# Kernel optimization log

Measured on AMD Instinct MI355X. Metric: run time of the kernel, lower is better.

Reference implementation:

```python
import jax, jax.numpy as jnp
import numpy as np

N = 50000
E = 800000
T = 5            # towers
F = 10           # in_num / F_in per tower (divide_input=False)
F_OUT = 2        # out_channels // towers
G = 64           # number of graphs in the batch
L = 2            # conv layers
BN_EPS = 1e-5
STD_EPS = 1e-5


def setup_inputs() -> dict:
    key = jax.random.key(0)
    ks = jax.random.split(key, 24)
    s = 0.1
    inp = {
        'x': jax.random.normal(ks[0], (N, F), jnp.float32),
        'edge_emb': jax.random.normal(ks[1], (4, F), jnp.float32) * s,
        'mlp1_w1': jax.random.normal(ks[2], (F, 5), jnp.float32) * s,
        'mlp1_b1': jnp.zeros((5,), jnp.float32),
        'mlp1_w2': jax.random.normal(ks[3], (5, F), jnp.float32) * s,
        'mlp1_b2': jnp.zeros((F,), jnp.float32),
        'enc_w': jax.random.normal(ks[4], (L, F, F), jnp.float32) * s,
        'enc_b': jnp.zeros((L, F), jnp.float32),
        'pre_w': jax.random.normal(ks[5], (L, T, 3 * F, F), jnp.float32) * s,
        'pre_b': jnp.zeros((L, T, F), jnp.float32),
        'post_w': jax.random.normal(ks[6], (L, T, 13 * F, F_OUT), jnp.float32) * s,
        'post_b': jnp.zeros((L, T, F_OUT), jnp.float32),
        'lin_w': jax.random.normal(ks[7], (L, F, F), jnp.float32) * s,
        'lin_b': jnp.zeros((L, F), jnp.float32),
        'bn_gamma': jnp.ones((L, F), jnp.float32),
        'bn_beta': jnp.zeros((L, F), jnp.float32),
        'mlp2_w1': jax.random.normal(ks[8], (F, 5), jnp.float32) * s,
        'mlp2_b1': jnp.zeros((5,), jnp.float32),
        'mlp2_w2': jax.random.normal(ks[9], (5, 1), jnp.float32) * s,
        'mlp2_b2': jnp.zeros((1,), jnp.float32),
        'edge_index': jax.random.randint(ks[10], (2, E), 0, N, jnp.int64),
        'edge_attr': jax.random.randint(ks[11], (E,), 0, 4, jnp.int64),
        'batch': jnp.sort(jax.random.randint(ks[12], (N,), 0, G, jnp.int64)),
    }
    return inp


def reference(x, edge_emb, mlp1_w1, mlp1_b1, mlp1_w2, mlp1_b2,
              enc_w, enc_b, pre_w, pre_b, post_w, post_b, lin_w, lin_b,
              bn_gamma, bn_beta, mlp2_w1, mlp2_b1, mlp2_w2, mlp2_b2,
              edge_index, edge_attr, batch):
    src, dst = edge_index[0], edge_index[1]
    # mlp1: 10 -> 5 -> 10
    h = jax.nn.relu(x @ mlp1_w1 + mlp1_b1) @ mlp1_w2 + mlp1_b2  # [N, F]
    ea = edge_emb[edge_attr]  # [E, F] edge embedding lookup

    # in-degree at target nodes, PNA degree statistics
    deg = jax.ops.segment_sum(jnp.ones((src.shape[0],), h.dtype), dst, num_segments=N)
    d = jnp.clip(deg, 1.0)
    avg_log = jnp.mean(jnp.log(deg + 1.0))  # avg_deg['log'] from degree distribution
    log_d = jnp.log(d + 1.0)
    amp = (log_d / avg_log)[:, None, None]
    att = (avg_log / log_d)[:, None, None]
    has_in = (deg > 0)[:, None, None]
    inv_d = (1.0 / d)[:, None, None]

    for l in range(L):
        e = ea @ enc_w[l] + enc_b[l]  # [E, F]
        # message = pre_nn(cat(x_i, x_j, edge_attr)) per tower (x shared across towers)
        msg_in = jnp.concatenate([h[dst], h[src], e], axis=-1)  # [E, 3F]
        m = jnp.einsum('ef,tfo->eto', msg_in, pre_w[l]) + pre_b[l]  # [E, T, F]
        mean = jax.ops.segment_sum(m, dst, num_segments=N) * inv_d
        mean2 = jax.ops.segment_sum(m * m, dst, num_segments=N) * inv_d
        std = jnp.sqrt(jax.nn.relu(mean2 - mean * mean) + STD_EPS)
        mn = jnp.where(has_in, jax.ops.segment_min(m, dst, num_segments=N), 0.0)
        mx = jnp.where(has_in, jax.ops.segment_max(m, dst, num_segments=N), 0.0)
        agg = jnp.concatenate([mean, mn, mx, std], axis=-1)  # [N, T, 4F]
        agg = jnp.concatenate([agg, agg * amp, agg * att], axis=-1)  # [N, T, 12F]
        xt = jnp.broadcast_to(h[:, None, :], (h.shape[0], T, F))
        o = jnp.concatenate([xt, agg], axis=-1)  # [N, T, 13F]
        o = jnp.einsum('ntf,tfo->nto', o, post_w[l]) + post_b[l]  # [N, T, F_OUT]
        o = o.reshape(o.shape[0], T * F_OUT) @ lin_w[l] + lin_b[l]  # [N, F]
        # train-mode BatchNorm over nodes
        mu = jnp.mean(o, axis=0)
        var = jnp.var(o, axis=0)
        o = (o - mu) / jnp.sqrt(var + BN_EPS) * bn_gamma[l] + bn_beta[l]
        h = jax.nn.relu(o)

    g = jax.ops.segment_sum(h, batch, num_segments=G)  # global_add_pool -> [G, F]
    out = jax.nn.relu(g @ mlp2_w1 + mlp2_b1) @ mlp2_w2 + mlp2_b2  # [G, 1]
    return out
```

## Files before the change

kernel.cpp:

```cpp
#include <hip/hip_runtime.h>
#include <math.h>

#define N_NODES 50000
#define N_EDGES 800000
#define G_GRAPHS 64
#define CONV_BLOCKS 2048
#define BSTRIDE 64

#define WAVE_SYNC() asm volatile("s_waitcnt lgkmcnt(0)" ::: "memory")
#define RFL(v) __builtin_amdgcn_readfirstlane(v)

__global__ void k_mlp1(const float* __restrict__ x,
                       const float* __restrict__ w1, const float* __restrict__ b1,
                       const float* __restrict__ w2, const float* __restrict__ b2,
                       float* __restrict__ h,
                       int* __restrict__ cnt,
                       float* __restrict__ bn_part, float* __restrict__ g,
                       float* __restrict__ avg_log,
                       const float* __restrict__ edge_emb,
                       const float* __restrict__ enc_w, const float* __restrict__ enc_b,
                       const float* __restrict__ pre_w, float* __restrict__ encm,
                       float* __restrict__ u) {
  __shared__ float eo[2][4][10];
  __shared__ float sw[500];
  int tid = threadIdx.x;
  int n = blockIdx.x * blockDim.x + tid;
  if (n < 1280) bn_part[n] = 0.f;
  if (n < G_GRAPHS * 10) g[n] = 0.f;
  if (n == 0) avg_log[0] = 0.f;

  bool act = n < N_NODES;
  float hr[10];
  if (act) {
    cnt[n] = 0;
    float xv[10];
#pragma unroll
    for (int k = 0; k < 10; k++) xv[k] = x[n * 10 + k];
    float hid[5];
#pragma unroll
    for (int j = 0; j < 5; j++) {
      float a = b1[j];
#pragma unroll
      for (int k = 0; k < 10; k++) a += xv[k] * w1[k * 5 + j];
      hid[j] = fmaxf(a, 0.f);
    }
#pragma unroll
    for (int f = 0; f < 10; f++) {
      float a = b2[f];
#pragma unroll
      for (int j = 0; j < 5; j++) a += hid[j] * w2[j * 10 + f];
      hr[f] = a;
      h[n * 10 + f] = a;
    }
  }
  for (int j = tid; j < 500; j += 256) {
    int t = j / 100, k = (j / 10) % 10, f = j % 10;
    sw[j] = pre_w[(t * 30 + 10 + k) * 10 + f];
  }
  if (blockIdx.x == 0) {
    for (int i = tid; i < 80; i += 256) {
      int l = i / 40; int a = (i / 10) % 4; int k = i % 10;
      float s = enc_b[l * 10 + k];
      for (int j = 0; j < 10; j++) s += edge_emb[a * 10 + j] * enc_w[(l * 10 + j) * 10 + k];
      eo[l][a][k] = s;
    }
  }
  __syncthreads();
  if (blockIdx.x == 0) {
    for (int i = tid; i < 400; i += 256) {
      int l = i / 200; int a = (i / 50) % 4; int t = (i / 10) % 5; int f = i % 10;
      float s = 0.f;
      for (int k = 0; k < 10; k++) s += eo[l][a][k] * pre_w[((l * 5 + t) * 30 + 20 + k) * 10 + f];
      encm[i] = s;
    }
  }
  if (act) {
    float2* up = (float2*)(u + n * 50);
#pragma unroll
    for (int c0 = 0; c0 < 25; c0++) {
      int ca = 2 * c0, cb = 2 * c0 + 1;
      int ta = ca / 10, fa = ca % 10, tb = cb / 10, fb = cb % 10;
      float a = 0.f, b = 0.f;
#pragma unroll
      for (int k = 0; k < 10; k++) {
        a += hr[k] * sw[ta * 100 + fa + k * 10];
        b += hr[k] * sw[tb * 100 + fb + k * 10];
      }
      up[c0] = make_float2(a, b);
    }
  }
}

__global__ void k_scatter(const int* __restrict__ src, const int* __restrict__ dst,
                          const int* __restrict__ attr,
                          int* __restrict__ cnt, int* __restrict__ epk) {
  int e = blockIdx.x * blockDim.x + threadIdx.x;
  if (e >= N_EDGES) return;
  int d = dst[e];
  int s = src[e];
  int a = attr[e];
  int k = atomicAdd(&cnt[d], 1);
  if (k < BSTRIDE) epk[d * BSTRIDE + k] = s | (a << 16);
}

__global__ void k_avg(const int* __restrict__ cnt, float* __restrict__ avg_log) {
  __shared__ float ws[4];
  int tid = threadIdx.x;
  float acc = 0.f;
  for (int n = blockIdx.x * 256 + tid; n < N_NODES; n += gridDim.x * 256)
    acc += __logf((float)cnt[n] + 1.f);
#pragma unroll
  for (int d = 32; d >= 1; d >>= 1) acc += __shfl_down(acc, d, 64);
  if ((tid & 63) == 0) ws[tid >> 6] = acc;
  __syncthreads();
  if (tid == 0) atomicAdd(avg_log, ws[0] + ws[1] + ws[2] + ws[3]);
}

__global__ __launch_bounds__(256) void k_conv(
    const float* __restrict__ h,
    const float* __restrict__ u,
    const float* __restrict__ pre_w_l,
    const float* __restrict__ pre_b_l,
    const float* __restrict__ post_w_l,
    const float* __restrict__ post_b_l,
    const float* __restrict__ lin_w_l,
    const float* __restrict__ lin_b_l,
    const float* __restrict__ encm_l,
    const int* __restrict__ cnt,
    const int* __restrict__ epk,
    const float* __restrict__ avg_log_p,
    float* __restrict__ o_buf,
    float* __restrict__ bn_part)
{
  __shared__ float sW[1300];
  __shared__ float sLin[100];
  __shared__ float sLb[10];
  __shared__ float sPb[10];
  __shared__ float sP[4][100];
  __shared__ float sO[4][10];
  __shared__ float bnS[10], bnQ[10];

  int tid = threadIdx.x;
  int wid = tid >> 6, lane = tid & 63;
  for (int i = tid; i < 1300; i += 256) sW[i] = post_w_l[i];
  for (int i = tid; i < 100; i += 256) sLin[i] = lin_w_l[i];
  if (tid < 10) {
    sLb[tid] = lin_b_l[tid];
    sPb[tid] = post_b_l[tid];
    bnS[tid] = 0.f; bnQ[tid] = 0.f;
  }
  __syncthreads();

  int f = lane % 10;
  int t = (lane < 50) ? (lane / 10) : 4;
  int c50 = t * 10 + f;
  float wdst[10];
#pragma unroll
  for (int k = 0; k < 10; k++) wdst[k] = pre_w_l[(t * 30 + k) * 10 + f];
  float em0 = encm_l[c50];
  float em1 = encm_l[50 + c50];
  float em2 = encm_l[100 + c50];
  float em3 = encm_l[150 + c50];
  float preb = pre_b_l[c50];
  float avg_log = avg_log_p[0] * (1.f / N_NODES);

  int gw = blockIdx.x * 4 + wid;
  int GW = gridDim.x * 4;
  int nn = (gw < N_NODES) ? ((N_NODES - 1 - gw) / GW + 1) : 0;

  int dgp = 0;
  if (lane < nn) dgp = cnt[gw + lane * GW];

  float bnSv = 0.f, bnQv = 0.f;

#define PRE(US, AS, IDX) { int sp_ = __builtin_amdgcn_readlane(pk, (IDX) & 63); \
    AS = sp_ >> 16; US = 0.f; \
    if ((IDX) < deg) US = u[(sp_ & 0xFFFF) * 50 + c50]; }
#define PROC(US, AS) { float em_ = (AS & 2) ? ((AS & 1) ? em3 : em2) : ((AS & 1) ? em1 : em0); \
    float m_ = base + em_ + US; \
    sum += m_; sq = fmaf(m_, m_, sq); mnv = fminf(mnv, m_); mxv = fmaxf(mxv, m_); }

  int nxt_pk = 0;
  if (nn > 0) {
    int deg0 = RFL(__builtin_amdgcn_readlane(dgp, 0));
    if (deg0 > BSTRIDE) deg0 = BSTRIDE;
    if (lane < deg0) nxt_pk = epk[gw * BSTRIDE + lane];
  }

  for (int i = 0; i < nn; i++) {
    int n = gw + i * GW;
    int deg = RFL(__builtin_amdgcn_readlane(dgp, i));
    if (deg > BSTRIDE) deg = BSTRIDE;
    int pk = nxt_pk;
    if (i + 1 < nn) {
      int degN = RFL(__builtin_amdgcn_readlane(dgp, i + 1));
      if (degN > BSTRIDE) degN = BSTRIDE;
      int nN = gw + (i + 1) * GW;
      nxt_pk = (lane < degN) ? epk[nN * BSTRIDE + lane] : 0;
    }

    const float* hn = h + n * 10;
    float2 d0 = *(const float2*)hn;
    float2 d1 = *(const float2*)(hn + 2);
    float2 d2 = *(const float2*)(hn + 4);
    float2 d3 = *(const float2*)(hn + 6);
    float2 d4 = *(const float2*)(hn + 8);
    float xf = hn[f];
    float base = preb
      + d0.x * wdst[0] + d0.y * wdst[1] + d1.x * wdst[2] + d1.y * wdst[3]
      + d2.x * wdst[4] + d2.y * wdst[5] + d3.x * wdst[6] + d3.y * wdst[7]
      + d4.x * wdst[8] + d4.y * wdst[9];

    float sum = 0.f, sq = 0.f, mnv = INFINITY, mxv = -INFINITY;
    {
      float u0, u1, u2, u3, u4, u5, u6, u7;
      int a0, a1, a2, a3, a4, a5, a6, a7;
      PRE(u0, a0, 0) PRE(u1, a1, 1) PRE(u2, a2, 2) PRE(u3, a3, 3)
      PRE(u4, a4, 4) PRE(u5, a5, 5) PRE(u6, a6, 6) PRE(u7, a7, 7)
      int full = deg & ~7;
      int jb = 0;
      for (; jb < full; jb += 8) {
        PROC(u0, a0) PRE(u0, a0, jb + 8)
        PROC(u1, a1) PRE(u1, a1, jb + 9)
        PROC(u2, a2) PRE(u2, a2, jb + 10)
        PROC(u3, a3) PRE(u3, a3, jb + 11)
        PROC(u4, a4) PRE(u4, a4, jb + 12)
        PROC(u5, a5) PRE(u5, a5, jb + 13)
        PROC(u6, a6) PRE(u6, a6, jb + 14)
        PROC(u7, a7) PRE(u7, a7, jb + 15)
      }
      if (jb + 0 < deg) PROC(u0, a0)
      if (jb + 1 < deg) PROC(u1, a1)
      if (jb + 2 < deg) PROC(u2, a2)
      if (jb + 3 < deg) PROC(u3, a3)
      if (jb + 4 < deg) PROC(u4, a4)
      if (jb + 5 < deg) PROC(u5, a5)
      if (jb + 6 < deg) PROC(u6, a6)
    }

    float degf = (float)deg;
    float d = fmaxf(degf, 1.f);
    float inv = 1.f / d;
    float mean = sum * inv;
    float var = sq * inv - mean * mean;
    float stdv = sqrtf(fmaxf(var, 0.f) + 1e-5f);
    if (deg == 0) { mnv = 0.f; mxv = 0.f; }
    float log_d = logf(d + 1.f);
    float amp = log_d / avg_log;
    float att = avg_log / log_d;

    float vv[13];
    vv[0] = xf;
    vv[1] = mean;       vv[2] = mnv;        vv[3] = mxv;        vv[4] = stdv;
    vv[5] = mean * amp; vv[6] = mnv * amp;  vv[7] = mxv * amp;  vv[8] = stdv * amp;
    vv[9] = mean * att; vv[10] = mnv * att; vv[11] = mxv * att; vv[12] = stdv * att;
    float p0 = 0.f, p1 = 0.f;
#pragma unroll
    for (int j = 0; j < 13; j++) {
      const float2 w = *(const float2*)&sW[t * 260 + (f + 10 * j) * 2];
      p0 += vv[j] * w.x; p1 += vv[j] * w.y;
    }
    if (lane < 50) *(float2*)&sP[wid][c50 * 2] = make_float2(p0, p1);
    WAVE_SYNC();
    if (lane < 10) {
      int tt = lane >> 1, c = lane & 1;
      float o = sPb[lane];
#pragma unroll
      for (int ff = 0; ff < 10; ff++) o += sP[wid][(tt * 10 + ff) * 2 + c];
      sO[wid][lane] = o;
    }
    WAVE_SYNC();
    if (lane < 10) {
      float r = sLb[lane];
#pragma unroll
      for (int j = 0; j < 10; j++) r += sO[wid][j] * sLin[j * 10 + lane];
      o_buf[n * 10 + lane] = r;
      bnSv += r; bnQv += r * r;
    }
    WAVE_SYNC();
  }
#undef PRE
#undef PROC

  if (lane < 10) {
    atomicAdd(&bnS[lane], bnSv);
    atomicAdd(&bnQ[lane], bnQv);
  }
  __syncthreads();
  if (tid < 20) {
    float v = (tid < 10) ? bnS[tid] : bnQ[tid - 10];
    atomicAdd(&bn_part[(blockIdx.x & 31) * 20 + tid], v);
  }
}

__global__ __launch_bounds__(256) void k_bnpool(
    const float* __restrict__ o_buf,
    const float* __restrict__ bn_part,
    const float* __restrict__ gamma, const float* __restrict__ beta,
    float* __restrict__ h,
    const int* __restrict__ batch, float* __restrict__ g,
    const float* __restrict__ pre_w_next, float* __restrict__ u,
    int do_u, int do_pool) {
  __shared__ float sS[20];
  __shared__ float sMu[10], sInv[10];
  __shared__ float pool[8][10];
  __shared__ float hrow[25][10];
  __shared__ float sw[500];
  __shared__ int g0s;
  int tid = threadIdx.x;
  int n0 = blockIdx.x * 25;
  if (do_u) {
    for (int j = tid; j < 500; j += 256) {
      int t = j / 100, k = (j / 10) % 10, f = j % 10;
      sw[j] = pre_w_next[(t * 30 + 10 + k) * 10 + f];
    }
  }
  if (tid < 20) {
    float s = 0.f;
    for (int j = 0; j < 32; j++) s += bn_part[j * 20 + tid];
    sS[tid] = s;
  }
  if (tid < 80) pool[tid / 10][tid % 10] = 0.f;
  if (tid == 0) g0s = batch[n0];
  __syncthreads();
  if (tid < 10) {
    float mu = sS[tid] * (1.f / N_NODES);
    float var = sS[10 + tid] * (1.f / N_NODES) - mu * mu;
    sMu[tid] = mu;
    sInv[tid] = 1.f / sqrtf(fmaxf(var, 0.f) + 1e-5f);
  }
  __syncthreads();
  if (tid < 250) {
    int dn = tid / 10, f = tid % 10;
    int n = n0 + dn;
    int i = n * 10 + f;
    float o = (o_buf[i] - sMu[f]) * sInv[f] * gamma[f] + beta[f];
    float r = fmaxf(o, 0.f);
    h[i] = r;
    hrow[dn][f] = r;
    if (do_pool) {
      int dg = batch[n] - g0s;
      if (dg < 8) atomicAdd(&pool[dg][f], r);
      else atomicAdd(&g[(g0s + dg) * 10 + f], r);
    }
  }
  __syncthreads();
  if (do_u && tid < 250) {
#pragma unroll
    for (int it = 0; it < 5; it++) {
      int j = tid + it * 250;
      int node = j / 50, c = j % 50;
      int t = c / 10, f2 = c % 10;
      float acc = 0.f;
#pragma unroll
      for (int k = 0; k < 10; k++) acc += hrow[node][k] * sw[t * 100 + f2 + k * 10];
      u[n0 * 50 + j] = acc;
    }
  }
  if (do_pool) {
    __syncthreads();
    if (tid < 80) {
      float v = pool[tid / 10][tid % 10];
      if (v != 0.f) atomicAdd(&g[(g0s + tid / 10) * 10 + tid % 10], v);
    }
  }
}

__global__ void k_mlp2(const float* __restrict__ g,
                       const float* __restrict__ w1, const float* __restrict__ b1,
                       const float* __restrict__ w2, const float* __restrict__ b2,
                       float* __restrict__ out) {
  int b = threadIdx.x;
  if (b >= G_GRAPHS) return;
  float gv[10];
#pragma unroll
  for (int k = 0; k < 10; k++) gv[k] = g[b * 10 + k];
  float acc = b2[0];
#pragma unroll
  for (int j = 0; j < 5; j++) {
    float a = b1[j];
#pragma unroll
    for (int k = 0; k < 10; k++) a += gv[k] * w1[k * 5 + j];
    acc += fmaxf(a, 0.f) * w2[j];
  }
  out[b] = acc;
}

extern "C" void kernel_launch(void* const* d_in, const int* in_sizes, int n_in,
                              void* d_out, int out_size, void* d_ws, size_t ws_size,
                              hipStream_t stream) {
  const float* x        = (const float*)d_in[0];
  const float* edge_emb = (const float*)d_in[1];
  const float* m1w1 = (const float*)d_in[2];
  const float* m1b1 = (const float*)d_in[3];
  const float* m1w2 = (const float*)d_in[4];
  const float* m1b2 = (const float*)d_in[5];
  const float* enc_w = (const float*)d_in[6];
  const float* enc_b = (const float*)d_in[7];
  const float* pre_w = (const float*)d_in[8];
  const float* pre_b = (const float*)d_in[9];
  const float* post_w = (const float*)d_in[10];
  const float* post_b = (const float*)d_in[11];
  const float* lin_w = (const float*)d_in[12];
  const float* lin_b = (const float*)d_in[13];
  const float* bn_g = (const float*)d_in[14];
  const float* bn_b = (const float*)d_in[15];
  const float* m2w1 = (const float*)d_in[16];
  const float* m2b1 = (const float*)d_in[17];
  const float* m2w2 = (const float*)d_in[18];
  const float* m2b2 = (const float*)d_in[19];
  const int* edge_index = (const int*)d_in[20];
  const int* edge_attr  = (const int*)d_in[21];
  const int* batch      = (const int*)d_in[22];
  const int* src  = edge_index;
  const int* dstp = edge_index + N_EDGES;

  char* ws = (char*)d_ws;
  size_t off = 0;
  auto alloc = [&](size_t bytes) {
    void* p = ws + off;
    off += (bytes + 255) & ~(size_t)255;
    return p;
  };
  float*     h       = (float*)alloc(N_NODES * 10 * sizeof(float));
  float*     o_buf   = (float*)alloc(N_NODES * 10 * sizeof(float));
  float*     u       = (float*)alloc((size_t)(N_NODES * 50 + 64) * sizeof(float));
  int*       cnt     = (int*)alloc(N_NODES * sizeof(int));
  int*       epk     = (int*)alloc((size_t)N_NODES * BSTRIDE * sizeof(int));
  float*     encm    = (float*)alloc(400 * sizeof(float));
  float*     avg_log = (float*)alloc(16);
  float*     bn_part = (float*)alloc(2 * 32 * 20 * sizeof(float));
  float*     g       = (float*)alloc(G_GRAPHS * 10 * sizeof(float));

  k_mlp1<<<(N_NODES + 255) / 256, 256, 0, stream>>>(x, m1w1, m1b1, m1w2, m1b2, h,
                                                    cnt, bn_part, g, avg_log,
                                                    edge_emb, enc_w, enc_b, pre_w, encm, u);
  k_scatter<<<(N_EDGES + 255) / 256, 256, 0, stream>>>(src, dstp, edge_attr, cnt, epk);
  k_avg<<<64, 256, 0, stream>>>(cnt, avg_log);

  for (int l = 0; l < 2; l++) {
    k_conv<<<CONV_BLOCKS, 256, 0, stream>>>(
        h, u, pre_w + l * 1500, pre_b + l * 50, post_w + l * 1300, post_b + l * 10,
        lin_w + l * 100, lin_b + l * 10, encm + l * 200,
        cnt, epk, avg_log, o_buf, bn_part + l * 640);
    k_bnpool<<<N_NODES / 25, 256, 0, stream>>>(
        o_buf, bn_part + l * 640, bn_g + l * 10, bn_b + l * 10, h, batch, g,
        pre_w + 1500, u, l == 0, l == 1);
  }
  k_mlp2<<<1, 64, 0, stream>>>(g, m2w1, m2b1, m2w2, m2b2, (float*)d_out);
}
```

Baseline: 286.7 us.

## Replace per-node atomic edge scatter with two-pass coarse/fine bucketing

New measurement: 435.9 us. +52.1%, slower.

```diff
diff --git a/kernel.cpp b/kernel.cpp
--- a/kernel.cpp
+++ b/kernel.cpp
@@ -6,6 +6,8 @@
 #define G_GRAPHS 64
 #define CONV_BLOCKS 2048
 #define BSTRIDE 64
+#define NCB 196
+#define CCAP 1280
 
 #define WAVE_SYNC() asm volatile("s_waitcnt lgkmcnt(0)" ::: "memory")
 #define RFL(v) __builtin_amdgcn_readfirstlane(v)
@@ -14,7 +16,7 @@
                        const float* __restrict__ w1, const float* __restrict__ b1,
                        const float* __restrict__ w2, const float* __restrict__ b2,
                        float* __restrict__ h,
-                       int* __restrict__ cnt,
+                       int* __restrict__ bfill4,
                        float* __restrict__ bn_part, float* __restrict__ g,
                        float* __restrict__ avg_log,
                        const float* __restrict__ edge_emb,
@@ -27,12 +29,12 @@
   int n = blockIdx.x * blockDim.x + tid;
   if (n < 1280) bn_part[n] = 0.f;
   if (n < G_GRAPHS * 10) g[n] = 0.f;
+  if (n < NCB * 4) bfill4[n] = 0;
   if (n == 0) avg_log[0] = 0.f;
 
   bool act = n < N_NODES;
   float hr[10];
   if (act) {
-    cnt[n] = 0;
     float xv[10];
 #pragma unroll
     for (int k = 0; k < 10; k++) xv[k] = x[n * 10 + k];
@@ -91,29 +93,56 @@
   }
 }
 
-__global__ void k_scatter(const int* __restrict__ src, const int* __restrict__ dst,
-                          const int* __restrict__ attr,
-                          int* __restrict__ cnt, int* __restrict__ epk) {
+__global__ void k_coarse(const int* __restrict__ src, const int* __restrict__ dst,
+                         const int* __restrict__ attr,
+                         int* __restrict__ bfill4, int* __restrict__ coarse) {
   int e = blockIdx.x * blockDim.x + threadIdx.x;
   if (e >= N_EDGES) return;
   int d = dst[e];
   int s = src[e];
   int a = attr[e];
-  int k = atomicAdd(&cnt[d], 1);
-  if (k < BSTRIDE) epk[d * BSTRIDE + k] = s | (a << 16);
-}
-
-__global__ void k_avg(const int* __restrict__ cnt, float* __restrict__ avg_log) {
-  __shared__ float ws[4];
+  int cs = (d >> 8) * 4 + (e & 3);
+  int k = atomicAdd(&bfill4[cs], 1);
+  if (k < CCAP) coarse[cs * CCAP + k] = (d & 255) | (s << 8) | (a << 24);
+}
+
+__global__ __launch_bounds__(256) void k_fine(const int* __restrict__ bfill4,
+                                              const int* __restrict__ coarse,
+                                              int* __restrict__ epk,
+                                              int* __restrict__ cnt,
+                                              float* __restrict__ avg_log) {
+  __shared__ int lcnt[256];
+  __shared__ float wred[4];
   int tid = threadIdx.x;
-  float acc = 0.f;
-  for (int n = blockIdx.x * 256 + tid; n < N_NODES; n += gridDim.x * 256)
-    acc += __logf((float)cnt[n] + 1.f);
-#pragma unroll
-  for (int d = 32; d >= 1; d >>= 1) acc += __shfl_down(acc, d, 64);
-  if ((tid & 63) == 0) ws[tid >> 6] = acc;
-  __syncthreads();
-  if (tid == 0) atomicAdd(avg_log, ws[0] + ws[1] + ws[2] + ws[3]);
+  int b = blockIdx.x;
+  int n0 = b * 256;
+  lcnt[tid] = 0;
+  __syncthreads();
+#pragma unroll
+  for (int s = 0; s < 4; s++) {
+    int cs = b * 4 + s;
+    int len = bfill4[cs];
+    if (len > CCAP) len = CCAP;
+    const int* base = coarse + cs * CCAP;
+    for (int j = tid; j < len; j += 256) {
+      int rec = base[j];
+      int dlo = rec & 255;
+      int k = atomicAdd(&lcnt[dlo], 1);
+      if (k < BSTRIDE) epk[(n0 + dlo) * BSTRIDE + k] = rec >> 8;
+    }
+  }
+  __syncthreads();
+  int deg = lcnt[tid];
+  float lg = 0.f;
+  if (n0 + tid < N_NODES) {
+    cnt[n0 + tid] = deg;
+    lg = __logf((float)deg + 1.f);
+  }
+#pragma unroll
+  for (int d = 32; d >= 1; d >>= 1) lg += __shfl_down(lg, d, 64);
+  if ((tid & 63) == 0) wred[tid >> 6] = lg;
+  __syncthreads();
+  if (tid == 0) atomicAdd(avg_log, wred[0] + wred[1] + wred[2] + wred[3]);
 }
 
 __global__ __launch_bounds__(256) void k_conv(
@@ -427,16 +456,18 @@
   float*     u       = (float*)alloc((size_t)(N_NODES * 50 + 64) * sizeof(float));
   int*       cnt     = (int*)alloc(N_NODES * sizeof(int));
   int*       epk     = (int*)alloc((size_t)N_NODES * BSTRIDE * sizeof(int));
+  int*       bfill4  = (int*)alloc(NCB * 4 * sizeof(int));
+  int*       coarse  = (int*)alloc((size_t)NCB * 4 * CCAP * sizeof(int));
   float*     encm    = (float*)alloc(400 * sizeof(float));
   float*     avg_log = (float*)alloc(16);
   float*     bn_part = (float*)alloc(2 * 32 * 20 * sizeof(float));
   float*     g       = (float*)alloc(G_GRAPHS * 10 * sizeof(float));
 
   k_mlp1<<<(N_NODES + 255) / 256, 256, 0, stream>>>(x, m1w1, m1b1, m1w2, m1b2, h,
-                                                    cnt, bn_part, g, avg_log,
+                                                    bfill4, bn_part, g, avg_log,
                                                     edge_emb, enc_w, enc_b, pre_w, encm, u);
-  k_scatter<<<(N_EDGES + 255) / 256, 256, 0, stream>>>(src, dstp, edge_attr, cnt, epk);
-  k_avg<<<64, 256, 0, stream>>>(cnt, avg_log);
+  k_coarse<<<(N_EDGES + 255) / 256, 256, 0, stream>>>(src, dstp, edge_attr, bfill4, coarse);
+  k_fine<<<NCB, 256, 0, stream>>>(bfill4, coarse, epk, cnt, avg_log);
 
   for (int l = 0; l < 2; l++) {
     k_conv<<<CONV_BLOCKS, 256, 0, stream>>>(
```

## Fuse edge scatter into mlp1 kernel and replicate global pool accumulators

Applied to the files above, without the earlier changes.

Result: slower. 296.3 us (+3.3%).

```diff
diff --git a/kernel.cpp b/kernel.cpp
--- a/kernel.cpp
+++ b/kernel.cpp
@@ -6,33 +6,51 @@
 #define G_GRAPHS 64
 #define CONV_BLOCKS 2048
 #define BSTRIDE 64
+#define NB_SC 3125
+#define NB_MLP 196
 
 #define WAVE_SYNC() asm volatile("s_waitcnt lgkmcnt(0)" ::: "memory")
 #define RFL(v) __builtin_amdgcn_readfirstlane(v)
 
-__global__ void k_mlp1(const float* __restrict__ x,
-                       const float* __restrict__ w1, const float* __restrict__ b1,
-                       const float* __restrict__ w2, const float* __restrict__ b2,
-                       float* __restrict__ h,
-                       int* __restrict__ cnt,
-                       float* __restrict__ bn_part, float* __restrict__ g,
-                       float* __restrict__ avg_log,
-                       const float* __restrict__ edge_emb,
-                       const float* __restrict__ enc_w, const float* __restrict__ enc_b,
-                       const float* __restrict__ pre_w, float* __restrict__ encm,
-                       float* __restrict__ u) {
+__global__ __launch_bounds__(256) void k_mlp1s(
+    const float* __restrict__ x,
+    const float* __restrict__ w1, const float* __restrict__ b1,
+    const float* __restrict__ w2, const float* __restrict__ b2,
+    float* __restrict__ h,
+    int* __restrict__ cnt,
+    float* __restrict__ bn_part, float* __restrict__ g_rep,
+    float* __restrict__ avg_log,
+    const float* __restrict__ edge_emb,
+    const float* __restrict__ enc_w, const float* __restrict__ enc_b,
+    const float* __restrict__ pre_w, float* __restrict__ encm,
+    float* __restrict__ u,
+    const int* __restrict__ src, const int* __restrict__ dstp,
+    const int* __restrict__ attr, int* __restrict__ epk) {
   __shared__ float eo[2][4][10];
   __shared__ float sw[500];
+  __shared__ float hrow[256][10];
   int tid = threadIdx.x;
-  int n = blockIdx.x * blockDim.x + tid;
+
+  if (blockIdx.x < NB_SC) {
+    int e = blockIdx.x * 256 + tid;
+    if (e < N_EDGES) {
+      int d = dstp[e];
+      int s = src[e];
+      int a = attr[e];
+      int k = atomicAdd(&cnt[d], 1);
+      if (k < BSTRIDE) epk[d * BSTRIDE + k] = s | (a << 16);
+    }
+    return;
+  }
+
+  int mblk = blockIdx.x - NB_SC;
+  int n = mblk * 256 + tid;
   if (n < 1280) bn_part[n] = 0.f;
-  if (n < G_GRAPHS * 10) g[n] = 0.f;
+  if (n < 32 * G_GRAPHS * 10) g_rep[n] = 0.f;
   if (n == 0) avg_log[0] = 0.f;
 
   bool act = n < N_NODES;
-  float hr[10];
   if (act) {
-    cnt[n] = 0;
     float xv[10];
 #pragma unroll
     for (int k = 0; k < 10; k++) xv[k] = x[n * 10 + k];
@@ -49,7 +67,7 @@
       float a = b2[f];
 #pragma unroll
       for (int j = 0; j < 5; j++) a += hid[j] * w2[j * 10 + f];
-      hr[f] = a;
+      hrow[tid][f] = a;
       h[n * 10 + f] = a;
     }
   }
@@ -57,7 +75,7 @@
     int t = j / 100, k = (j / 10) % 10, f = j % 10;
     sw[j] = pre_w[(t * 30 + 10 + k) * 10 + f];
   }
-  if (blockIdx.x == 0) {
+  if (mblk == 0) {
     for (int i = tid; i < 80; i += 256) {
       int l = i / 40; int a = (i / 10) % 4; int k = i % 10;
       float s = enc_b[l * 10 + k];
@@ -66,7 +84,7 @@
     }
   }
   __syncthreads();
-  if (blockIdx.x == 0) {
+  if (mblk == 0) {
     for (int i = tid; i < 400; i += 256) {
       int l = i / 200; int a = (i / 50) % 4; int t = (i / 10) % 5; int f = i % 10;
       float s = 0.f;
@@ -74,33 +92,17 @@
       encm[i] = s;
     }
   }
-  if (act) {
-    float2* up = (float2*)(u + n * 50);
-#pragma unroll
-    for (int c0 = 0; c0 < 25; c0++) {
-      int ca = 2 * c0, cb = 2 * c0 + 1;
-      int ta = ca / 10, fa = ca % 10, tb = cb / 10, fb = cb % 10;
-      float a = 0.f, b = 0.f;
-#pragma unroll
-      for (int k = 0; k < 10; k++) {
-        a += hr[k] * sw[ta * 100 + fa + k * 10];
-        b += hr[k] * sw[tb * 100 + fb + k * 10];
-      }
-      up[c0] = make_float2(a, b);
-    }
-  }
-}
-
-__global__ void k_scatter(const int* __restrict__ src, const int* __restrict__ dst,
-                          const int* __restrict__ attr,
-                          int* __restrict__ cnt, int* __restrict__ epk) {
-  int e = blockIdx.x * blockDim.x + threadIdx.x;
-  if (e >= N_EDGES) return;
-  int d = dst[e];
-  int s = src[e];
-  int a = attr[e];
-  int k = atomicAdd(&cnt[d], 1);
-  if (k < BSTRIDE) epk[d * BSTRIDE + k] = s | (a << 16);
+  int n0 = mblk * 256;
+  int nodesv = N_NODES - n0; if (nodesv > 256) nodesv = 256;
+  int jmax = nodesv * 50;
+  for (int j = tid; j < jmax; j += 256) {
+    int node = j / 50, c = j % 50;
+    int t = c / 10, f2 = c % 10;
+    float acc = 0.f;
+#pragma unroll
+    for (int k = 0; k < 10; k++) acc += hrow[node][k] * sw[t * 100 + f2 + k * 10];
+    u[(size_t)n0 * 50 + j] = acc;
+  }
 }
 
 __global__ void k_avg(const int* __restrict__ cnt, float* __restrict__ avg_log) {
@@ -298,7 +300,7 @@
     const float* __restrict__ bn_part,
     const float* __restrict__ gamma, const float* __restrict__ beta,
     float* __restrict__ h,
-    const int* __restrict__ batch, float* __restrict__ g,
+    const int* __restrict__ batch, float* __restrict__ g_rep,
     const float* __restrict__ pre_w_next, float* __restrict__ u,
     int do_u, int do_pool) {
   __shared__ float sS[20];
@@ -309,6 +311,7 @@
   __shared__ int g0s;
   int tid = threadIdx.x;
   int n0 = blockIdx.x * 25;
+  int rep = (blockIdx.x & 31) * G_GRAPHS * 10;
   if (do_u) {
     for (int j = tid; j < 500; j += 256) {
       int t = j / 100, k = (j / 10) % 10, f = j % 10;
@@ -341,7 +344,7 @@
     if (do_pool) {
       int dg = batch[n] - g0s;
       if (dg < 8) atomicAdd(&pool[dg][f], r);
-      else atomicAdd(&g[(g0s + dg) * 10 + f], r);
+      else atomicAdd(&g_rep[rep + (g0s + dg) * 10 + f], r);
     }
   }
   __syncthreads();
@@ -361,12 +364,12 @@
     __syncthreads();
     if (tid < 80) {
       float v = pool[tid / 10][tid % 10];
-      if (v != 0.f) atomicAdd(&g[(g0s + tid / 10) * 10 + tid % 10], v);
-    }
-  }
-}
-
-__global__ void k_mlp2(const float* __restrict__ g,
+      if (v != 0.f) atomicAdd(&g_rep[rep + (g0s + tid / 10) * 10 + tid % 10], v);
+    }
+  }
+}
+
+__global__ void k_mlp2(const float* __restrict__ g_rep,
                        const float* __restrict__ w1, const float* __restrict__ b1,
                        const float* __restrict__ w2, const float* __restrict__ b2,
                        float* __restrict__ out) {
@@ -374,7 +377,11 @@
   if (b >= G_GRAPHS) return;
   float gv[10];
 #pragma unroll
-  for (int k = 0; k < 10; k++) gv[k] = g[b * 10 + k];
+  for (int k = 0; k < 10; k++) gv[k] = 0.f;
+  for (int r = 0; r < 32; r++) {
+#pragma unroll
+    for (int k = 0; k < 10; k++) gv[k] += g_rep[r * G_GRAPHS * 10 + b * 10 + k];
+  }
   float acc = b2[0];
 #pragma unroll
   for (int j = 0; j < 5; j++) {
@@ -430,12 +437,14 @@
   float*     encm    = (float*)alloc(400 * sizeof(float));
   float*     avg_log = (float*)alloc(16);
   float*     bn_part = (float*)alloc(2 * 32 * 20 * sizeof(float));
-  float*     g       = (float*)alloc(G_GRAPHS * 10 * sizeof(float));
-
-  k_mlp1<<<(N_NODES + 255) / 256, 256, 0, stream>>>(x, m1w1, m1b1, m1w2, m1b2, h,
-                                                    cnt, bn_part, g, avg_log,
-                                                    edge_emb, enc_w, enc_b, pre_w, encm, u);
-  k_scatter<<<(N_EDGES + 255) / 256, 256, 0, stream>>>(src, dstp, edge_attr, cnt, epk);
+  float*     g_rep   = (float*)alloc(32 * G_GRAPHS * 10 * sizeof(float));
+
+  hipMemsetAsync(cnt, 0, N_NODES * sizeof(int), stream);
+
+  k_mlp1s<<<NB_SC + NB_MLP, 256, 0, stream>>>(x, m1w1, m1b1, m1w2, m1b2, h,
+                                              cnt, bn_part, g_rep, avg_log,
+                                              edge_emb, enc_w, enc_b, pre_w, encm, u,
+                                              src, dstp, edge_attr, epk);
   k_avg<<<64, 256, 0, stream>>>(cnt, avg_log);
 
   for (int l = 0; l < 2; l++) {
@@ -444,8 +453,8 @@
         lin_w + l * 100, lin_b + l * 10, encm + l * 200,
         cnt, epk, avg_log, o_buf, bn_part + l * 640);
     k_bnpool<<<N_NODES / 25, 256, 0, stream>>>(
-        o_buf, bn_part + l * 640, bn_g + l * 10, bn_b + l * 10, h, batch, g,
+        o_buf, bn_part + l * 640, bn_g + l * 10, bn_b + l * 10, h, batch, g_rep,
         pre_w + 1500, u, l == 0, l == 1);
   }
-  k_mlp2<<<1, 64, 0, stream>>>(g, m2w1, m2b1, m2w2, m2b2, (float*)d_out);
-}
+  k_mlp2<<<1, 64, 0, stream>>>(g_rep, m2w1, m2b1, m2w2, m2b2, (float*)d_out);
+}
```
